# Kernel tuning notes

Measured on AMD Instinct MI355X. Metric: run time of the kernel, lower is better.

## Reference

```python
import jax, jax.numpy as jnp
import numpy as np

N_ITERS = 200  # matches maxIter=200 in the original QPFunction


def setup_inputs() -> dict:
    key = jax.random.key(0)
    k1, k2, k3 = jax.random.split(key, 3)
    B, M, N = 8192, 128, 64
    A = jax.random.normal(k1, (B, M, N), dtype=jnp.float32)
    x = jax.random.normal(k2, (B, N), dtype=jnp.float32)
    # b > 0 guarantees z = 0 is feasible for A z <= b, so every instance is solvable
    b = jax.random.uniform(k3, (B, M), dtype=jnp.float32)
    Q = jnp.eye(N, dtype=jnp.float32)  # module parameter: self.Q = diag(ones(feature_size))
    return {"Q": Q, "A": A, "x": x, "b": b}


def reference(Q, A, x, b):
    """Batched QP:  min_z 1/2 z^T Q z - x^T z  s.t.  A z <= b.

    Solved via FISTA (accelerated projected gradient ascent) on the dual:
        max_{lam >= 0}  -1/2 (x - A^T lam)^T Q^{-1} (x - A^T lam) - lam^T b + const
    Primal recovery: z = Q^{-1} (x - A^T lam).
    Fully batched and jit-friendly (fixed N_ITERS, lax.scan).
    """
    Qinv = jnp.linalg.inv(Q)  # [n, n], tiny

    # Lipschitz bound for dual gradient: ||A Qinv A^T||_2 <= ||A||_F^2 * ||Qinv||_F
    L = jnp.sum(A * A, axis=(1, 2)) * jnp.linalg.norm(Qinv)  # [B]
    eta = jax.lax.stop_gradient(1.0 / jnp.maximum(L, 1e-12))[:, None]  # [B, 1]

    def primal(lam):
        # z = Qinv (x - A^T lam), shape [B, n]
        return jnp.einsum('nk,bk->bn', Qinv, x - jnp.einsum('bmn,bm->bn', A, lam))

    def step(carry, _):
        lam, y, t = carry
        z = primal(y)                                   # [B, n]
        g = jnp.einsum('bmn,bn->bm', A, z) - b          # dual gradient A z - b, [B, m]
        lam_new = jax.nn.relu(y + eta * g)              # projected ascent step
        t_new = 0.5 * (1.0 + jnp.sqrt(1.0 + 4.0 * t * t))
        y_new = lam_new + ((t - 1.0) / t_new) * (lam_new - lam)
        return (lam_new, y_new, t_new), None

    lam0 = jnp.zeros_like(b)
    t0 = jnp.float32(1.0)
    (lam, _, _), _ = jax.lax.scan(step, (lam0, lam0, t0), None, length=N_ITERS)
    return primal(lam)  # optimal z, [B, n]
```

## Files before the change

### kernel.cpp

```cpp
#include <hip/hip_runtime.h>


constexpr double csqrt_(double x) {
  double g = x * 0.5 + 0.5;
  for (int i = 0; i < 40; ++i) g = 0.5 * (g + x / g);
  return g;
}
struct CoefT { float c[200]; };
constexpr CoefT make_coefs() {
  CoefT T{};
  double t = 1.0;
  for (int k = 0; k < 200; ++k) {
    double tn = 0.5 * (1.0 + csqrt_(1.0 + 4.0 * t * t));
    T.c[k] = (float)((t - 1.0) / tn);
    t = tn;
  }
  return T;
}
__device__ constexpr CoefT kCoef = make_coefs();

__device__ __forceinline__ float dpp_add_xor1(float v) {
  int r = __builtin_amdgcn_update_dpp(0, __float_as_int(v), 0xB1, 0xF, 0xF, true);
  return v + __int_as_float(r);
}
__device__ __forceinline__ float dpp_add_xor2(float v) {
  int r = __builtin_amdgcn_update_dpp(0, __float_as_int(v), 0x4E, 0xF, 0xF, true);
  return v + __int_as_float(r);
}
__device__ __forceinline__ float swz_add_xor4(float v) {
  int r = __builtin_amdgcn_ds_swizzle(__float_as_int(v), 0x101F);
  return v + __int_as_float(r);
}

__global__ __launch_bounds__(512)
void qp_fista_kernel(const float* __restrict__ A,
                     const float* __restrict__ x,
                     const float* __restrict__ b,
                     float* __restrict__ out) {
  const int batch = blockIdx.x;
  const int tid = threadIdx.x;
  const int w = tid >> 6;

  __shared__ __align__(16) float tile[8192];

  const float* Ag = A + (size_t)batch * 8192;

  {
    const float4* Ag4 = (const float4*)Ag;
    float4* t4 = (float4*)tile;
#pragma unroll
    for (int k = 0; k < 4; ++k) t4[tid + k * 512] = Ag4[tid + k * 512];
  }
  __syncthreads();

  const int r  = tid >> 2;
  const int cq = tid & 3;
  float Ar[16];
  {
    const float4* t4 = (const float4*)tile;
#pragma unroll
    for (int j = 0; j < 4; ++j) {
      float4 v = t4[r * 16 + cq * 4 + j];
      Ar[4 * j + 0] = v.x; Ar[4 * j + 1] = v.y;
      Ar[4 * j + 2] = v.z; Ar[4 * j + 3] = v.w;
    }
  }
  const int c  = tid >> 3;
  const int rq = tid & 7;
  float Ac[16];
#pragma unroll
  for (int i = 0; i < 16; ++i) Ac[i] = tile[(rq * 16 + i) * 64 + c];

  float ss = 0.f;
#pragma unroll
  for (int i = 0; i < 16; ++i) ss = fmaf(Ar[i], Ar[i], ss);
#pragma unroll
  for (int d = 1; d < 64; d <<= 1) ss += __shfl_xor(ss, d, 64);

  __syncthreads();

  float* zbuf = tile;
  float* ybuf = tile + 96;
  float* wsb  = tile + 272;
  unsigned* wflag = (unsigned*)(tile + 288);

  if ((tid & 63) == 0) wsb[w] = ss;
  const float breg = b[(size_t)batch * 128 + r];
  const float xreg = x[(size_t)batch * 64 + c];
  if (rq == 0) zbuf[(c >> 4) * 20 + (c & 15)] = xreg;
  __syncthreads();

  float sum8 = 0.f;
#pragma unroll
  for (int i = 0; i < 8; ++i) sum8 += wsb[i];
  const float eta = 1.0f / fmaxf(8.0f * sum8, 1e-12f);

  const float4* zs = (const float4*)(zbuf + cq * 20);
  const float4* ys = (const float4*)(ybuf + rq * 20);
  float* ywr = ybuf + (w) * 20 + (r & 15);
  float* zwr = zbuf + (c >> 4) * 20 + (c & 15);

  float lam = 0.f, y = 0.f;

#pragma unroll 1
  for (int it = 0; it < 199; ++it) {
    const float coef = kCoef.c[it];

    float p0 = 0.f, p1 = 0.f;
#pragma unroll
    for (int j = 0; j < 4; ++j) {
      float4 zz = zs[j];
      p0 = fmaf(Ar[4 * j + 0], zz.x, p0);
      p1 = fmaf(Ar[4 * j + 1], zz.y, p1);
      p0 = fmaf(Ar[4 * j + 2], zz.z, p0);
      p1 = fmaf(Ar[4 * j + 3], zz.w, p1);
    }
    float acc = p0 + p1;
    acc = dpp_add_xor1(acc);
    acc = dpp_add_xor2(acc);
    float g  = acc - breg;
    float ln = fmaxf(0.f, fmaf(eta, g, y));
    float yn = fmaf(coef, ln - lam, ln);

    if ((it & 3) == 3) {
      bool changed = (ln != y) || (yn != y);
      unsigned long long bal = __ballot(changed);
      if ((tid & 63) == 0) wflag[w] = (bal != 0ull) ? 1u : 0u;
    }
    lam = ln; y = yn;
    if (cq == 0) *ywr = yn;
    __syncthreads();

    if ((it & 3) == 3) {
      const uint4* f4 = (const uint4*)wflag;
      uint4 f0 = f4[0], f1 = f4[1];
      if (!(f0.x | f0.y | f0.z | f0.w | f1.x | f1.y | f1.z | f1.w))
        goto early_done;
    }

    float q0 = 0.f, q1 = 0.f;
#pragma unroll
    for (int j = 0; j < 4; ++j) {
      float4 yy = ys[j];
      q0 = fmaf(Ac[4 * j + 0], yy.x, q0);
      q1 = fmaf(Ac[4 * j + 1], yy.y, q1);
      q0 = fmaf(Ac[4 * j + 2], yy.z, q0);
      q1 = fmaf(Ac[4 * j + 3], yy.w, q1);
    }
    float s = q0 + q1;
    s = dpp_add_xor1(s);
    s = dpp_add_xor2(s);
    s = swz_add_xor4(s);
    if (rq == 0) *zwr = xreg - s;
    __syncthreads();
  }

  {
    float p0 = 0.f, p1 = 0.f;
#pragma unroll
    for (int j = 0; j < 4; ++j) {
      float4 zz = zs[j];
      p0 = fmaf(Ar[4 * j + 0], zz.x, p0);
      p1 = fmaf(Ar[4 * j + 1], zz.y, p1);
      p0 = fmaf(Ar[4 * j + 2], zz.z, p0);
      p1 = fmaf(Ar[4 * j + 3], zz.w, p1);
    }
    float acc = p0 + p1;
    acc = dpp_add_xor1(acc);
    acc = dpp_add_xor2(acc);
    float g  = acc - breg;
    float ln = fmaxf(0.f, fmaf(eta, g, y));
    if (cq == 0) *ywr = ln;
    __syncthreads();

    float q0 = 0.f, q1 = 0.f;
#pragma unroll
    for (int j = 0; j < 4; ++j) {
      float4 yy = ys[j];
      q0 = fmaf(Ac[4 * j + 0], yy.x, q0);
      q1 = fmaf(Ac[4 * j + 1], yy.y, q1);
      q0 = fmaf(Ac[4 * j + 2], yy.z, q0);
      q1 = fmaf(Ac[4 * j + 3], yy.w, q1);
    }
    float s = q0 + q1;
    s = dpp_add_xor1(s);
    s = dpp_add_xor2(s);
    s = swz_add_xor4(s);
    if (rq == 0) *zwr = xreg - s;
    __syncthreads();
  }

early_done:
  if (tid < 64) {
    out[(size_t)batch * 64 + tid] = zbuf[(tid >> 4) * 20 + (tid & 15)];
  }
}

extern "C" void kernel_launch(void* const* d_in, const int* in_sizes, int n_in,
                              void* d_out, int out_size, void* d_ws, size_t ws_size,
                              hipStream_t stream) {
  const float* A = (const float*)d_in[1];
  const float* x = (const float*)d_in[2];
  const float* b = (const float*)d_in[3];
  float* out = (float*)d_out;
  qp_fista_kernel<<<dim3(8192), dim3(512), 0, stream>>>(A, x, b, out);
}
```

Baseline: 1.145 ms.

## Precompute Gram matrix A·A^T and iterate the dual in lambda space

```diff
diff --git a/kernel.cpp b/kernel.cpp
--- a/kernel.cpp
+++ b/kernel.cpp
@@ -39,9 +39,19 @@
                      float* __restrict__ out) {
   const int batch = blockIdx.x;
   const int tid = threadIdx.x;
-  const int w = tid >> 6;
-
-  __shared__ __align__(16) float tile[8192];
+  const int w  = tid >> 6;
+  const int r  = tid >> 2;
+  const int cq = tid & 3;
+  const int c  = tid >> 3;
+  const int rq = tid & 7;
+
+  __shared__ __align__(16) float tile[8736];
+  float* xsec = tile + 8192;
+  float* yA   = tile + 8272;
+  float* yB   = tile + 8416;
+  float* lamS = tile + 8560;
+  float* wsb  = tile + 8720;
+  unsigned* wflag = (unsigned*)(tile + 8728);
 
   const float* Ag = A + (size_t)batch * 8192;
 
@@ -51,43 +61,47 @@
 #pragma unroll
     for (int k = 0; k < 4; ++k) t4[tid + k * 512] = Ag4[tid + k * 512];
   }
+  if (tid < 64) xsec[(tid >> 4) * 20 + (tid & 15)] = x[(size_t)batch * 64 + tid];
+  if (tid < 144) yA[tid] = 0.f;
+  const float breg = b[(size_t)batch * 128 + r];
+  const float xreg = x[(size_t)batch * 64 + c];
   __syncthreads();
 
-  const int r  = tid >> 2;
-  const int cq = tid & 3;
-  float Ar[16];
+  float Arq[16];
   {
     const float4* t4 = (const float4*)tile;
 #pragma unroll
     for (int j = 0; j < 4; ++j) {
       float4 v = t4[r * 16 + cq * 4 + j];
-      Ar[4 * j + 0] = v.x; Ar[4 * j + 1] = v.y;
-      Ar[4 * j + 2] = v.z; Ar[4 * j + 3] = v.w;
-    }
-  }
-  const int c  = tid >> 3;
-  const int rq = tid & 7;
-  float Ac[16];
-#pragma unroll
-  for (int i = 0; i < 16; ++i) Ac[i] = tile[(rq * 16 + i) * 64 + c];
+      Arq[4 * j + 0] = v.x; Arq[4 * j + 1] = v.y;
+      Arq[4 * j + 2] = v.z; Arq[4 * j + 3] = v.w;
+    }
+  }
 
   float ss = 0.f;
 #pragma unroll
-  for (int i = 0; i < 16; ++i) ss = fmaf(Ar[i], Ar[i], ss);
+  for (int i = 0; i < 16; ++i) ss = fmaf(Arq[i], Arq[i], ss);
 #pragma unroll
   for (int d = 1; d < 64; d <<= 1) ss += __shfl_xor(ss, d, 64);
-
-  __syncthreads();
-
-  float* zbuf = tile;
-  float* ybuf = tile + 96;
-  float* wsb  = tile + 272;
-  unsigned* wflag = (unsigned*)(tile + 288);
-
   if ((tid & 63) == 0) wsb[w] = ss;
-  const float breg = b[(size_t)batch * 128 + r];
-  const float xreg = x[(size_t)batch * 64 + c];
-  if (rq == 0) zbuf[(c >> 4) * 20 + (c & 15)] = xreg;
+
+  float c0r;
+  {
+    const float4* xq = (const float4*)(xsec + cq * 20);
+    float p0 = 0.f, p1 = 0.f;
+#pragma unroll
+    for (int s4 = 0; s4 < 4; ++s4) {
+      float4 v = xq[s4];
+      p0 = fmaf(Arq[4 * s4 + 0], v.x, p0);
+      p1 = fmaf(Arq[4 * s4 + 1], v.y, p1);
+      p0 = fmaf(Arq[4 * s4 + 2], v.z, p0);
+      p1 = fmaf(Arq[4 * s4 + 3], v.w, p1);
+    }
+    float axr = p0 + p1;
+    axr = dpp_add_xor1(axr);
+    axr = dpp_add_xor2(axr);
+    c0r = axr - breg;
+  }
   __syncthreads();
 
   float sum8 = 0.f;
@@ -95,104 +109,115 @@
   for (int i = 0; i < 8; ++i) sum8 += wsb[i];
   const float eta = 1.0f / fmaxf(8.0f * sum8, 1e-12f);
 
-  const float4* zs = (const float4*)(zbuf + cq * 20);
-  const float4* ys = (const float4*)(ybuf + rq * 20);
-  float* ywr = ybuf + (w) * 20 + (r & 15);
-  float* zwr = zbuf + (c >> 4) * 20 + (c & 15);
-
+  float Greg[32];
+#pragma unroll
+  for (int u = 0; u < 32; ++u) Greg[u] = 0.f;
+#pragma unroll 1
+  for (int cch = 0; cch < 4; ++cch) {
+    const bool keep = (cq == cch);
+    const float* Abase = tile + cch * 2048 + cq * 16;
+#pragma unroll
+    for (int jj = 0; jj < 32; ++jj) {
+      const float4* Aj = (const float4*)(Abase + jj * 64);
+      float g0 = 0.f, g1 = 0.f;
+#pragma unroll
+      for (int s4 = 0; s4 < 4; ++s4) {
+        float4 v = Aj[s4];
+        g0 = fmaf(Arq[4 * s4 + 0], v.x, g0);
+        g1 = fmaf(Arq[4 * s4 + 1], v.y, g1);
+        g0 = fmaf(Arq[4 * s4 + 2], v.z, g0);
+        g1 = fmaf(Arq[4 * s4 + 3], v.w, g1);
+      }
+      float gf = g0 + g1;
+      gf = dpp_add_xor1(gf);
+      gf = dpp_add_xor2(gf);
+      Greg[jj] = keep ? gf : Greg[jj];
+    }
+  }
+
+  const int cq36 = cq * 36;
+  const int wr_off = (r >> 5) * 36 + (r & 31);
+  const bool iswr = (cq == 0);
   float lam = 0.f, y = 0.f;
 
 #pragma unroll 1
-  for (int it = 0; it < 199; ++it) {
-    const float coef = kCoef.c[it];
-
-    float p0 = 0.f, p1 = 0.f;
-#pragma unroll
-    for (int j = 0; j < 4; ++j) {
-      float4 zz = zs[j];
-      p0 = fmaf(Ar[4 * j + 0], zz.x, p0);
-      p1 = fmaf(Ar[4 * j + 1], zz.y, p1);
-      p0 = fmaf(Ar[4 * j + 2], zz.z, p0);
-      p1 = fmaf(Ar[4 * j + 3], zz.w, p1);
-    }
-    float acc = p0 + p1;
-    acc = dpp_add_xor1(acc);
-    acc = dpp_add_xor2(acc);
-    float g  = acc - breg;
-    float ln = fmaxf(0.f, fmaf(eta, g, y));
-    float yn = fmaf(coef, ln - lam, ln);
-
-    if ((it & 3) == 3) {
-      bool changed = (ln != y) || (yn != y);
-      unsigned long long bal = __ballot(changed);
-      if ((tid & 63) == 0) wflag[w] = (bal != 0ull) ? 1u : 0u;
-    }
-    lam = ln; y = yn;
-    if (cq == 0) *ywr = yn;
-    __syncthreads();
-
-    if ((it & 3) == 3) {
-      const uint4* f4 = (const uint4*)wflag;
-      uint4 f0 = f4[0], f1 = f4[1];
-      if (!(f0.x | f0.y | f0.z | f0.w | f1.x | f1.y | f1.z | f1.w))
-        goto early_done;
-    }
-
-    float q0 = 0.f, q1 = 0.f;
-#pragma unroll
-    for (int j = 0; j < 4; ++j) {
-      float4 yy = ys[j];
-      q0 = fmaf(Ac[4 * j + 0], yy.x, q0);
-      q1 = fmaf(Ac[4 * j + 1], yy.y, q1);
-      q0 = fmaf(Ac[4 * j + 2], yy.z, q0);
-      q1 = fmaf(Ac[4 * j + 3], yy.w, q1);
-    }
-    float s = q0 + q1;
+  for (int kk = 0; kk < 100; ++kk) {
+    {
+      const float4* yq = (const float4*)(yA + cq36);
+      float q0 = 0.f, q1 = 0.f;
+#pragma unroll
+      for (int u = 0; u < 8; ++u) {
+        float4 v = yq[u];
+        q0 = fmaf(Greg[4 * u + 0], v.x, q0);
+        q1 = fmaf(Greg[4 * u + 1], v.y, q1);
+        q0 = fmaf(Greg[4 * u + 2], v.z, q0);
+        q1 = fmaf(Greg[4 * u + 3], v.w, q1);
+      }
+      float acc = q0 + q1;
+      acc = dpp_add_xor1(acc);
+      acc = dpp_add_xor2(acc);
+      float ln = fmaxf(0.f, fmaf(eta, c0r - acc, y));
+      float yn = fmaf(kCoef.c[2 * kk], ln - lam, ln);
+      lam = ln; y = yn;
+      if (iswr) yB[wr_off] = yn;
+      __syncthreads();
+    }
+    {
+      const float4* yq = (const float4*)(yB + cq36);
+      float q0 = 0.f, q1 = 0.f;
+#pragma unroll
+      for (int u = 0; u < 8; ++u) {
+        float4 v = yq[u];
+        q0 = fmaf(Greg[4 * u + 0], v.x, q0);
+        q1 = fmaf(Greg[4 * u + 1], v.y, q1);
+        q0 = fmaf(Greg[4 * u + 2], v.z, q0);
+        q1 = fmaf(Greg[4 * u + 3], v.w, q1);
+      }
+      float acc = q0 + q1;
+      acc = dpp_add_xor1(acc);
+      acc = dpp_add_xor2(acc);
+      float ln = fmaxf(0.f, fmaf(eta, c0r - acc, y));
+      float yn = fmaf(kCoef.c[2 * kk + 1], ln - lam, ln);
+      const bool probe = ((kk & 3) == 3);
+      if (probe) {
+        bool chg = (ln != y) || (yn != y);
+        unsigned long long bal = __ballot(chg);
+        if ((tid & 63) == 0) wflag[w] = (bal != 0ull) ? 1u : 0u;
+      }
+      lam = ln; y = yn;
+      if (iswr) yA[wr_off] = yn;
+      __syncthreads();
+      if (probe) {
+        const uint4* f4 = (const uint4*)wflag;
+        uint4 f0 = f4[0], f1 = f4[1];
+        if (!(f0.x | f0.y | f0.z | f0.w | f1.x | f1.y | f1.z | f1.w))
+          goto fista_done;
+      }
+    }
+  }
+
+fista_done:
+  if (iswr) lamS[(r >> 4) * 20 + (r & 15)] = lam;
+  __syncthreads();
+  {
+    float Acc[16];
+#pragma unroll
+    for (int i = 0; i < 16; ++i) Acc[i] = tile[(rq * 16 + i) * 64 + c];
+    const float4* ls = (const float4*)(lamS + rq * 20);
+    float s0 = 0.f, s1 = 0.f;
+#pragma unroll
+    for (int s4 = 0; s4 < 4; ++s4) {
+      float4 v = ls[s4];
+      s0 = fmaf(Acc[4 * s4 + 0], v.x, s0);
+      s1 = fmaf(Acc[4 * s4 + 1], v.y, s1);
+      s0 = fmaf(Acc[4 * s4 + 2], v.z, s0);
+      s1 = fmaf(Acc[4 * s4 + 3], v.w, s1);
+    }
+    float s = s0 + s1;
     s = dpp_add_xor1(s);
     s = dpp_add_xor2(s);
     s = swz_add_xor4(s);
-    if (rq == 0) *zwr = xreg - s;
-    __syncthreads();
-  }
-
-  {
-    float p0 = 0.f, p1 = 0.f;
-#pragma unroll
-    for (int j = 0; j < 4; ++j) {
-      float4 zz = zs[j];
-      p0 = fmaf(Ar[4 * j + 0], zz.x, p0);
-      p1 = fmaf(Ar[4 * j + 1], zz.y, p1);
-      p0 = fmaf(Ar[4 * j + 2], zz.z, p0);
-      p1 = fmaf(Ar[4 * j + 3], zz.w, p1);
-    }
-    float acc = p0 + p1;
-    acc = dpp_add_xor1(acc);
-    acc = dpp_add_xor2(acc);
-    float g  = acc - breg;
-    float ln = fmaxf(0.f, fmaf(eta, g, y));
-    if (cq == 0) *ywr = ln;
-    __syncthreads();
-
-    float q0 = 0.f, q1 = 0.f;
-#pragma unroll
-    for (int j = 0; j < 4; ++j) {
-      float4 yy = ys[j];
-      q0 = fmaf(Ac[4 * j + 0], yy.x, q0);
-      q1 = fmaf(Ac[4 * j + 1], yy.y, q1);
-      q0 = fmaf(Ac[4 * j + 2], yy.z, q0);
-      q1 = fmaf(Ac[4 * j + 3], yy.w, q1);
-    }
-    float s = q0 + q1;
-    s = dpp_add_xor1(s);
-    s = dpp_add_xor2(s);
-    s = swz_add_xor4(s);
-    if (rq == 0) *zwr = xreg - s;
-    __syncthreads();
-  }
-
-early_done:
-  if (tid < 64) {
-    out[(size_t)batch * 64 + tid] = zbuf[(tid >> 4) * 20 + (tid & 15)];
+    if (rq == 0) out[(size_t)batch * 64 + c] = xreg - s;
   }
 }
 
```

After: 1.514 ms. +32.2%, slower.
